# Kernel optimization log

Hardware: AMD Instinct MI355X
Metric: run time of the kernel (lower is better)

Reference implementation:

```python
import jax, jax.numpy as jnp
import numpy as np

B = 128          # batch of trees (same topology)
N_LEAVES = 512
N_NODES = 2 * N_LEAVES - 1   # 1023, null child slot = N_NODES
IN_DIM = 300
MEM_DIM = 300


def _build_tree():
    # complete binary tree, level order: leaves first, then parents.
    null = N_NODES
    left = [null] * N_LEAVES
    right = [null] * N_LEAVES
    prev = list(range(N_LEAVES))
    nid = N_LEAVES
    while len(prev) > 1:
        cur = []
        for k in range(0, len(prev), 2):
            left.append(prev[k]); right.append(prev[k + 1])
            cur.append(nid); nid += 1
        prev = cur
    left = np.asarray(left, np.int32)
    right = np.asarray(right, np.int32)
    leaf_mask = (left == null).astype(np.int32)
    return left, right, leaf_mask


def setup_inputs() -> dict:
    key = jax.random.key(0)
    ks = jax.random.split(key, 5)
    left, right, leaf_mask = _build_tree()
    s = 0.05  # keep gates out of saturation
    return {
        "inputs": jax.random.normal(ks[0], (B, N_NODES, IN_DIM), jnp.float32),
        "Wfioux": jax.random.normal(ks[1], (IN_DIM, 4 * MEM_DIM), jnp.float32) * s,
        "b_fioux": jax.random.normal(ks[2], (4 * MEM_DIM,), jnp.float32) * s,
        "Wiouh": jax.random.normal(ks[3], (2 * MEM_DIM, 3 * MEM_DIM), jnp.float32) * s,
        "Wfh": jax.random.normal(ks[4], (2 * MEM_DIM, 2 * MEM_DIM), jnp.float32) * s,
        "left_idx": jnp.asarray(left),
        "right_idx": jnp.asarray(right),
        "leaf_mask": jnp.asarray(leaf_mask),
    }


def _tree_lstm(inputs, Wfioux, b_fioux, Wiouh, Wfh, left_idx, right_idx, leaf_mask):
    b, n, _ = inputs.shape
    mem = Wiouh.shape[1] // 3
    # internal nodes get zero input (as in the torch code)
    x = inputs * leaf_mask.astype(inputs.dtype)[None, :, None]
    # input-dependent gates precomputed for all nodes: [n, b, 4*mem]
    fioux = jnp.einsum('bni,io->nbo', x, Wfioux) + b_fioux

    C0 = jnp.zeros((n + 1, b, mem), inputs.dtype)  # row n = null child = zeros
    H0 = jnp.zeros((n + 1, b, mem), inputs.dtype)

    def step(carry, xs):
        C, H = carry
        i, li, ri, fioux_i = xs
        ch_c = jnp.concatenate([C[li], C[ri]], axis=-1)  # [b, 2*mem]
        ch_h = jnp.concatenate([H[li], H[ri]], axis=-1)
        fx, ix, ox, ux = jnp.split(fioux_i, 4, axis=-1)
        ih, oh, uh = jnp.split(ch_h @ Wiouh, 3, axis=-1)
        i_g = jax.nn.sigmoid(ix + ih)
        o_g = jax.nn.sigmoid(ox + oh)
        u_g = jnp.tanh(ux + uh)
        f_g = jax.nn.sigmoid(jnp.tile(fx, (1, 2)) + ch_h @ Wfh)
        fc = (f_g * ch_c).reshape(b, 2, mem).sum(axis=1)
        c = i_g * u_g + fc
        h = o_g * jnp.tanh(c)
        return (C.at[li * 0 + i].set(c), H.at[i].set(h)), None

    xs = (jnp.arange(n, dtype=jnp.int32), left_idx, right_idx, fioux)
    (C, H), _ = jax.lax.scan(step, (C0, H0), xs)
    return C[n - 1], H[n - 1]  # root state (c, h), each [b, mem]


def reference(inputs, Wfioux, b_fioux, Wiouh, Wfh, left_idx, right_idx, leaf_mask):
    return _tree_lstm(inputs, Wfioux, b_fioux, Wiouh, Wfh, left_idx, right_idx, leaf_mask)
```

## Files before the change

kernel.cpp:

```cpp
#include <hip/hip_runtime.h>
#include <cstdint>

#define BATCH 128
#define NODES 1023
#define LEAVES 512
#define IN_DIM 300
#define MEM 300
#define NP 320
#define OUT_HALF (BATCH*MEM)

typedef __bf16   bf16x8 __attribute__((ext_vector_type(8)));
typedef short    s16x8  __attribute__((ext_vector_type(8)));
typedef short    s16x4  __attribute__((ext_vector_type(4)));
typedef float    f32x4  __attribute__((ext_vector_type(4)));
typedef _Float16 half_t;

__device__ __forceinline__ short f2bf(float f) {
    unsigned u = __float_as_uint(f);
    u += 0x7fff + ((u >> 16) & 1);
    return (short)(u >> 16);
}
__device__ __forceinline__ float sigf(float x)  { return 1.0f / (1.0f + __expf(-x)); }
__device__ __forceinline__ float tanhf_(float x){ return 1.0f - 2.0f / (1.0f + __expf(2.0f * x)); }

__device__ __forceinline__ f32x4 mfma16(s16x8 a, s16x8 b, f32x4 c) {
    return __builtin_amdgcn_mfma_f32_16x16x32_bf16(
        __builtin_bit_cast(bf16x8, a), __builtin_bit_cast(bf16x8, b), c, 0, 0, 0);
}

__device__ __forceinline__ void dma16(const short* src, short* ldsBase) {
    __builtin_amdgcn_global_load_lds(
        (const __attribute__((address_space(1))) unsigned int*)src,
        (__attribute__((address_space(3))) unsigned int*)ldsBase,
        16, 0, 0);
}

__global__ __launch_bounds__(256) void pack_node_w(
    const float* __restrict__ Wiouh, const float* __restrict__ Wfh, short* __restrict__ Wpk)
{
    int gid = blockIdx.x * 256 + threadIdx.x;
    if (gid >= 2000 * 64) return;
    int fb = gid >> 6, l = gid & 63;
    int kb = fb / 100, rem = fb % 100, s = rem / 20, nb = rem % 20;
    int n = nb * 16 + (l & 15);
    int kbase = kb * 32 + (l >> 4) * 8;
    short v[8];
#pragma unroll
    for (int j = 0; j < 8; ++j) {
        int kp = kbase + j;
        int side = kp >= NP;
        int kk = kp - side * NP;
        float f = 0.0f;
        if (kk < MEM && n < MEM) {
            int k = side * MEM + kk;
            f = (s < 3) ? Wiouh[(size_t)k * 900 + s * 300 + n]
                        : Wfh[(size_t)k * 600 + (s - 3) * 300 + n];
        }
        v[j] = f2bf(f);
    }
    *(s16x8*)&Wpk[(size_t)gid * 8] = *(s16x8*)v;
}

__global__ __launch_bounds__(256) void pack_leaf_w(
    const float* __restrict__ Wfioux, short* __restrict__ Wpk)
{
    int gid = blockIdx.x * 256 + threadIdx.x;
    if (gid >= 600 * 64) return;
    int fb = gid >> 6, l = gid & 63;
    int kb = fb / 60, rem = fb % 60, s = rem / 20, nb = rem % 20;
    int n = nb * 16 + (l & 15);
    int kbase = kb * 32 + (l >> 4) * 8;
    short v[8];
#pragma unroll
    for (int j = 0; j < 8; ++j) {
        int kp = kbase + j;
        float f = 0.0f;
        if (kp < IN_DIM && n < MEM)
            f = Wfioux[(size_t)kp * 1200 + (s + 1) * 300 + n];
        v[j] = f2bf(f);
    }
    *(s16x8*)&Wpk[(size_t)gid * 8] = *(s16x8*)v;
}

__global__ __launch_bounds__(256) void pack_x(
    const float* __restrict__ inputs, short* __restrict__ X)
{
    int gid = blockIdx.x * 256 + threadIdx.x;
    if (gid >= LEAVES * BATCH * (NP / 4)) return;
    int q = gid % (NP / 4);
    int rb = gid / (NP / 4);
    int b = rb % BATCH, leaf = rb / BATCH;
    short v[4] = {0, 0, 0, 0};
    if (q < IN_DIM / 4) {
        f32x4 f = *(const f32x4*)&inputs[((size_t)b * NODES + leaf) * IN_DIM + q * 4];
        v[0] = f2bf(f[0]); v[1] = f2bf(f[1]); v[2] = f2bf(f[2]); v[3] = f2bf(f[3]);
    }
    *(s16x4*)&X[(size_t)gid * 4] = *(s16x4*)v;
}

__global__ __launch_bounds__(256, 3) void leaf_mfma(
    const short* __restrict__ X, const short* __restrict__ Wpk,
    const float* __restrict__ b_fioux, half_t* __restrict__ C, short* __restrict__ H)
{
    __shared__ short Bs[4][12 * 512];
    const int t = threadIdx.x;
    const int l = t & 63, w = t >> 6;
    const int lane16 = l & 15, quad = l >> 4;

    const int bid = blockIdx.x;
    const int xcd = bid & 7, tt = bid >> 3;
    const int y = tt % 5;
    const int leaf = (tt / 5) * 8 + xcd;

    const short* Xb = X + (size_t)leaf * BATCH * NP;

    f32x4 acc[3][4][2];
#pragma unroll
    for (int s = 0; s < 3; ++s)
#pragma unroll
        for (int f = 0; f < 4; ++f)
#pragma unroll
            for (int mi = 0; mi < 2; ++mi) acc[s][f][mi] = (f32x4)(0.0f);

    s16x8 A[4][2];

#define L_STAGE(KB, BUF) do {                                                    \
    _Pragma("unroll")                                                            \
    for (int fl = w; fl < 12; fl += 4) {                                         \
        int s_ = fl >> 2, f_ = fl & 3;                                           \
        const short* src_ = Wpk +                                                \
            ((size_t)(((KB) * 3 + s_) * 20 + y * 4 + f_) * 64 + l) * 8;          \
        dma16(src_, &Bs[BUF][fl * 512]);                                         \
    } } while (0)

#define L_ALOAD(KB, SLOT) do {                                                   \
    const int koff_ = (KB) * 32 + quad * 8;                                      \
    A[SLOT][0] = *(const s16x8*)(Xb + (size_t)(w * 32 + lane16) * NP + koff_);   \
    A[SLOT][1] = *(const s16x8*)(Xb + (size_t)(w * 32 + 16 + lane16) * NP + koff_); \
} while (0)

    L_STAGE(0, 0); L_ALOAD(0, 0);
    L_STAGE(1, 1); L_ALOAD(1, 1);
    L_STAGE(2, 2); L_ALOAD(2, 2);

#define L_STEP(ST, WAITN) do {                                                   \
    asm volatile("s_waitcnt vmcnt(" #WAITN ")" ::: "memory");                    \
    __builtin_amdgcn_s_barrier();                                                \
    asm volatile("" ::: "memory");                                               \
    if ((ST) + 3 < 10) { L_STAGE((ST) + 3, ((ST) + 3) & 3);                      \
                         L_ALOAD((ST) + 3, ((ST) + 3) & 3); }                    \
    _Pragma("unroll")                                                            \
    for (int s_ = 0; s_ < 3; ++s_) {                                             \
        _Pragma("unroll")                                                        \
        for (int f_ = 0; f_ < 4; ++f_) {                                         \
            s16x8 b_ = *(const s16x8*)&Bs[(ST) & 3][(s_ * 4 + f_) * 512 + l * 8];\
            acc[s_][f_][0] = mfma16(A[(ST) & 3][0], b_, acc[s_][f_][0]);         \
            acc[s_][f_][1] = mfma16(A[(ST) & 3][1], b_, acc[s_][f_][1]);         \
        }                                                                        \
    } } while (0)

    L_STEP(0, 10); L_STEP(1, 10); L_STEP(2, 10); L_STEP(3, 10); L_STEP(4, 10);
    L_STEP(5, 10); L_STEP(6, 10); L_STEP(7, 10); L_STEP(8, 5);  L_STEP(9, 0);

#undef L_STEP
#undef L_ALOAD
#undef L_STAGE

#pragma unroll
    for (int f = 0; f < 4; ++f) {
        const int col = y * 64 + f * 16 + lane16;
        const bool valid = col < MEM;
        float bi = 0, bo = 0, bu = 0;
        if (valid) { bi = b_fioux[300 + col]; bo = b_fioux[600 + col]; bu = b_fioux[900 + col]; }
#pragma unroll
        for (int mi = 0; mi < 2; ++mi)
#pragma unroll
            for (int r = 0; r < 4; ++r) {
                int b = w * 32 + mi * 16 + quad * 4 + r;
                size_t hIdx = ((size_t)leaf * BATCH + b) * NP + col;
                if (valid) {
                    float ig = sigf(acc[0][f][mi][r] + bi);
                    float og = sigf(acc[1][f][mi][r] + bo);
                    float ug = tanhf_(acc[2][f][mi][r] + bu);
                    float c = ig * ug;
                    float h = og * tanhf_(c);
                    C[((size_t)leaf * BATCH + b) * MEM + col] = (half_t)c;
                    H[hIdx] = f2bf(h);
                } else {
                    H[hIdx] = 0;
                }
            }
    }
}

__global__ __launch_bounds__(256, 3) void node_mfma(
    const short* __restrict__ Wpk, const float* __restrict__ b_fioux,
    const int* __restrict__ left_idx, const int* __restrict__ right_idx,
    half_t* __restrict__ C, short* __restrict__ H,
    int level_start, int level_size, float* __restrict__ out)
{
    __shared__ short Bs[4][12 * 512];
    const int t = threadIdx.x;
    const int l = t & 63, w = t >> 6;
    const int lane16 = l & 15, quad = l >> 4;

    const int bid = blockIdx.x;
    int nidx, y;
    if ((level_size & 7) == 0) {
        const int xcd = bid & 7, tt = bid >> 3;
        y = tt % 10;
        nidx = (tt / 10) * 8 + xcd;
    } else {
        nidx = bid % level_size;
        y = bid / level_size;
    }
    const int node = level_start + nidx;

    const int li = left_idx[node], ri = right_idx[node];
    const short* HL = H + (size_t)li * BATCH * NP;
    const short* HR = H + (size_t)ri * BATCH * NP;

    f32x4 acc[5][2][2];
#pragma unroll
    for (int s = 0; s < 5; ++s)
#pragma unroll
        for (int f = 0; f < 2; ++f)
#pragma unroll
            for (int mi = 0; mi < 2; ++mi) acc[s][f][mi] = (f32x4)(0.0f);

    s16x8 A[4][2];

#define N_STAGE(KB, BUF) do {                                                    \
    _Pragma("unroll")                                                            \
    for (int fl = w; fl < 12; fl += 4) {                                         \
        int rfl_ = (fl < 10) ? fl : fl - 10;               \
        int s_ = rfl_ >> 1, f_ = rfl_ & 1;                                       \
        const short* src_ = Wpk +                                                \
            ((size_t)(((KB) * 5 + s_) * 20 + y * 2 + f_) * 64 + l) * 8;          \
        dma16(src_, &Bs[BUF][fl * 512]);                                         \
    } } while (0)

#define N_ALOAD(KB, SLOT) do {                                                   \
    const short* Hb_ = (((KB) >= 10) ? HR : HL) +                                \
                       ((KB) - (((KB) >= 10) ? 10 : 0)) * 32 + quad * 8;         \
    A[SLOT][0] = *(const s16x8*)(Hb_ + (size_t)(w * 32 + lane16) * NP);          \
    A[SLOT][1] = *(const s16x8*)(Hb_ + (size_t)(w * 32 + 16 + lane16) * NP);     \
} while (0)

    N_STAGE(0, 0); N_ALOAD(0, 0);
    N_STAGE(1, 1); N_ALOAD(1, 1);
    N_STAGE(2, 2); N_ALOAD(2, 2);

#define N_STEP(ST, WAITN) do {                                                   \
    asm volatile("s_waitcnt vmcnt(" #WAITN ")" ::: "memory");                    \
    __builtin_amdgcn_s_barrier();                                                \
    asm volatile("" ::: "memory");                                               \
    if ((ST) + 3 < 20) { N_STAGE((ST) + 3, ((ST) + 3) & 3);                      \
                         N_ALOAD((ST) + 3, ((ST) + 3) & 3); }                    \
    _Pragma("unroll")                                                            \
    for (int s_ = 0; s_ < 5; ++s_) {                                             \
        _Pragma("unroll")                                                        \
        for (int f_ = 0; f_ < 2; ++f_) {                                         \
            s16x8 b_ = *(const s16x8*)&Bs[(ST) & 3][(s_ * 2 + f_) * 512 + l * 8];\
            acc[s_][f_][0] = mfma16(A[(ST) & 3][0], b_, acc[s_][f_][0]);         \
            acc[s_][f_][1] = mfma16(A[(ST) & 3][1], b_, acc[s_][f_][1]);         \
        }                                                                        \
    } } while (0)

    N_STEP(0, 10);  N_STEP(1, 10);  N_STEP(2, 10);  N_STEP(3, 10);  N_STEP(4, 10);
    N_STEP(5, 10);  N_STEP(6, 10);  N_STEP(7, 10);  N_STEP(8, 10);  N_STEP(9, 10);
    N_STEP(10, 10); N_STEP(11, 10); N_STEP(12, 10); N_STEP(13, 10); N_STEP(14, 10);
    N_STEP(15, 10); N_STEP(16, 10); N_STEP(17, 10); N_STEP(18, 5);  N_STEP(19, 0);

#undef N_STEP
#undef N_ALOAD
#undef N_STAGE

#pragma unroll
    for (int f = 0; f < 2; ++f) {
        const int col = y * 32 + f * 16 + lane16;
        const bool valid = col < MEM;
        float bff = 0, bi = 0, bo = 0, bu = 0;
        if (valid) {
            bff = b_fioux[col]; bi = b_fioux[300 + col];
            bo = b_fioux[600 + col]; bu = b_fioux[900 + col];
        }
#pragma unroll
        for (int mi = 0; mi < 2; ++mi)
#pragma unroll
            for (int r = 0; r < 4; ++r) {
                int row = w * 32 + mi * 16 + quad * 4 + r;
                size_t hIdx = ((size_t)node * BATCH + row) * NP + col;
                if (valid) {
                    float cl = (float)C[((size_t)li * BATCH + row) * MEM + col];
                    float cr = (float)C[((size_t)ri * BATCH + row) * MEM + col];
                    float ig = sigf(acc[0][f][mi][r] + bi);
                    float og = sigf(acc[1][f][mi][r] + bo);
                    float ug = tanhf_(acc[2][f][mi][r] + bu);
                    float fl = sigf(acc[3][f][mi][r] + bff);
                    float fr = sigf(acc[4][f][mi][r] + bff);
                    float c = ig * ug + fl * cl + fr * cr;
                    float h = og * tanhf_(c);
                    C[((size_t)node * BATCH + row) * MEM + col] = (half_t)c;
                    H[hIdx] = f2bf(h);
                    if (out) {
                        out[row * MEM + col] = c;
                        out[OUT_HALF + row * MEM + col] = h;
                    }
                } else {
                    H[hIdx] = 0;
                }
            }
    }
}

extern "C" void kernel_launch(void* const* d_in, const int* in_sizes, int n_in,
                              void* d_out, int out_size, void* d_ws, size_t ws_size,
                              hipStream_t stream) {
    const float* inputs  = (const float*)d_in[0];
    const float* Wfioux  = (const float*)d_in[1];
    const float* b_fioux = (const float*)d_in[2];
    const float* Wiouh   = (const float*)d_in[3];
    const float* Wfh     = (const float*)d_in[4];
    const int*   left_idx  = (const int*)d_in[5];
    const int*   right_idx = (const int*)d_in[6];

    half_t* C   = (half_t*)d_ws;
    short*  H   = (short*)(C + (size_t)NODES * BATCH * MEM);
    short* WpkN = H + (size_t)NODES * BATCH * NP;
    short* WpkL = WpkN + (size_t)2000 * 512;
    short* X    = WpkL + (size_t)600 * 512;
    float* out  = (float*)d_out;

    pack_x<<<(LEAVES * BATCH * (NP / 4) + 255) / 256, 256, 0, stream>>>(inputs, X);
    pack_leaf_w<<<150, 256, 0, stream>>>(Wfioux, WpkL);
    pack_node_w<<<500, 256, 0, stream>>>(Wiouh, Wfh, WpkN);

    leaf_mfma<<<LEAVES * 5, 256, 0, stream>>>(X, WpkL, b_fioux, C, H);

    static const int starts[9] = {512, 768, 896, 960, 992, 1008, 1016, 1020, 1022};
    static const int sizes [9] = {256, 128,  64,  32,  16,    8,    4,    2,    1};
    for (int lvl = 0; lvl < 9; ++lvl) {
        bool root = (lvl == 8);
        node_mfma<<<sizes[lvl] * 10, 256, 0, stream>>>(
            WpkN, b_fioux, left_idx, right_idx, C, H, starts[lvl], sizes[lvl],
            root ? out : nullptr);
    }
}
```

Measured before the change: 627.8 us.

## Split waves 2x2 over rows and columns, shorten A-fragment prefetch depth

Each kernel's four waves are rearranged from four row-slices (each covering all columns) into a 2x2 grid: each wave now handles 64 batch rows and half of the block's columns. Each wave therefore reads half as many B fragments from LDS per MFMA but loads twice as many A rows from global memory. The A-operand global prefetch drops from three stages ahead to one (double buffer), while the LDS weight staging keeps three stages ahead, and the vmcnt wait counts are retuned to match. This is meant to cut LDS read traffic and register pressure, at the risk of exposing more global load latency on the A operand.

Result: slower. 798.2 us (+27.1%).

```diff
diff --git a/kernel.cpp b/kernel.cpp
--- a/kernel.cpp
+++ b/kernel.cpp
@@ -106,6 +106,7 @@
     const int t = threadIdx.x;
     const int l = t & 63, w = t >> 6;
     const int lane16 = l & 15, quad = l >> 4;
+    const int mw = w >> 1, nw = w & 1;
 
     const int bid = blockIdx.x;
     const int xcd = bid & 7, tt = bid >> 3;
@@ -114,15 +115,15 @@
 
     const short* Xb = X + (size_t)leaf * BATCH * NP;
 
-    f32x4 acc[3][4][2];
+    f32x4 acc[3][2][4];
 #pragma unroll
     for (int s = 0; s < 3; ++s)
 #pragma unroll
-        for (int f = 0; f < 4; ++f)
-#pragma unroll
-            for (int mi = 0; mi < 2; ++mi) acc[s][f][mi] = (f32x4)(0.0f);
-
-    s16x8 A[4][2];
+        for (int fh = 0; fh < 2; ++fh)
+#pragma unroll
+            for (int rh = 0; rh < 4; ++rh) acc[s][fh][rh] = (f32x4)(0.0f);
+
+    s16x8 A[2][4];
 
 #define L_STAGE(KB, BUF) do {                                                    \
     _Pragma("unroll")                                                            \
@@ -135,53 +136,56 @@
 
 #define L_ALOAD(KB, SLOT) do {                                                   \
     const int koff_ = (KB) * 32 + quad * 8;                                      \
-    A[SLOT][0] = *(const s16x8*)(Xb + (size_t)(w * 32 + lane16) * NP + koff_);   \
-    A[SLOT][1] = *(const s16x8*)(Xb + (size_t)(w * 32 + 16 + lane16) * NP + koff_); \
+    _Pragma("unroll")                                                            \
+    for (int rh_ = 0; rh_ < 4; ++rh_)                                            \
+        A[SLOT][rh_] = *(const s16x8*)(Xb +                                      \
+            (size_t)(mw * 64 + rh_ * 16 + lane16) * NP + koff_);                 \
 } while (0)
 
-    L_STAGE(0, 0); L_ALOAD(0, 0);
-    L_STAGE(1, 1); L_ALOAD(1, 1);
-    L_STAGE(2, 2); L_ALOAD(2, 2);
+    L_ALOAD(0, 0);
+    L_STAGE(0, 0); L_STAGE(1, 1); L_STAGE(2, 2);
 
 #define L_STEP(ST, WAITN) do {                                                   \
     asm volatile("s_waitcnt vmcnt(" #WAITN ")" ::: "memory");                    \
     __builtin_amdgcn_s_barrier();                                                \
     asm volatile("" ::: "memory");                                               \
-    if ((ST) + 3 < 10) { L_STAGE((ST) + 3, ((ST) + 3) & 3);                      \
-                         L_ALOAD((ST) + 3, ((ST) + 3) & 3); }                    \
+    if ((ST) + 1 < 10) L_ALOAD((ST) + 1, ((ST) + 1) & 1);                        \
+    if ((ST) + 3 < 10) L_STAGE((ST) + 3, ((ST) + 3) & 3);                        \
     _Pragma("unroll")                                                            \
     for (int s_ = 0; s_ < 3; ++s_) {                                             \
         _Pragma("unroll")                                                        \
-        for (int f_ = 0; f_ < 4; ++f_) {                                         \
-            s16x8 b_ = *(const s16x8*)&Bs[(ST) & 3][(s_ * 4 + f_) * 512 + l * 8];\
-            acc[s_][f_][0] = mfma16(A[(ST) & 3][0], b_, acc[s_][f_][0]);         \
-            acc[s_][f_][1] = mfma16(A[(ST) & 3][1], b_, acc[s_][f_][1]);         \
+        for (int fh_ = 0; fh_ < 2; ++fh_) {                                      \
+            s16x8 b_ = *(const s16x8*)                                           \
+                &Bs[(ST) & 3][(s_ * 4 + nw * 2 + fh_) * 512 + l * 8];            \
+            _Pragma("unroll")                                                    \
+            for (int rh_ = 0; rh_ < 4; ++rh_)                                    \
+                acc[s_][fh_][rh_] = mfma16(A[(ST) & 1][rh_], b_, acc[s_][fh_][rh_]); \
         }                                                                        \
     } } while (0)
 
-    L_STEP(0, 10); L_STEP(1, 10); L_STEP(2, 10); L_STEP(3, 10); L_STEP(4, 10);
-    L_STEP(5, 10); L_STEP(6, 10); L_STEP(7, 10); L_STEP(8, 5);  L_STEP(9, 0);
+    L_STEP(0, 6); L_STEP(1, 3); L_STEP(2, 3); L_STEP(3, 3); L_STEP(4, 3);
+    L_STEP(5, 3); L_STEP(6, 3); L_STEP(7, 3); L_STEP(8, 0); L_STEP(9, 0);
 
 #undef L_STEP
 #undef L_ALOAD
 #undef L_STAGE
 
 #pragma unroll
-    for (int f = 0; f < 4; ++f) {
-        const int col = y * 64 + f * 16 + lane16;
+    for (int fh = 0; fh < 2; ++fh) {
+        const int col = y * 64 + (nw * 2 + fh) * 16 + lane16;
         const bool valid = col < MEM;
         float bi = 0, bo = 0, bu = 0;
         if (valid) { bi = b_fioux[300 + col]; bo = b_fioux[600 + col]; bu = b_fioux[900 + col]; }
 #pragma unroll
-        for (int mi = 0; mi < 2; ++mi)
+        for (int rh = 0; rh < 4; ++rh)
 #pragma unroll
             for (int r = 0; r < 4; ++r) {
-                int b = w * 32 + mi * 16 + quad * 4 + r;
+                int b = mw * 64 + rh * 16 + quad * 4 + r;
                 size_t hIdx = ((size_t)leaf * BATCH + b) * NP + col;
                 if (valid) {
-                    float ig = sigf(acc[0][f][mi][r] + bi);
-                    float og = sigf(acc[1][f][mi][r] + bo);
-                    float ug = tanhf_(acc[2][f][mi][r] + bu);
+                    float ig = sigf(acc[0][fh][rh][r] + bi);
+                    float og = sigf(acc[1][fh][rh][r] + bo);
+                    float ug = tanhf_(acc[2][fh][rh][r] + bu);
                     float c = ig * ug;
                     float h = og * tanhf_(c);
                     C[((size_t)leaf * BATCH + b) * MEM + col] = (half_t)c;
@@ -203,6 +207,7 @@
     const int t = threadIdx.x;
     const int l = t & 63, w = t >> 6;
     const int lane16 = l & 15, quad = l >> 4;
+    const int mw = w >> 1, nw = w & 1;
 
     const int bid = blockIdx.x;
     int nidx, y;
@@ -220,15 +225,13 @@
     const short* HL = H + (size_t)li * BATCH * NP;
     const short* HR = H + (size_t)ri * BATCH * NP;
 
-    f32x4 acc[5][2][2];
+    f32x4 acc[5][4];
 #pragma unroll
     for (int s = 0; s < 5; ++s)
 #pragma unroll
-        for (int f = 0; f < 2; ++f)
-#pragma unroll
-            for (int mi = 0; mi < 2; ++mi) acc[s][f][mi] = (f32x4)(0.0f);
-
-    s16x8 A[4][2];
+        for (int rh = 0; rh < 4; ++rh) acc[s][rh] = (f32x4)(0.0f);
+
+    s16x8 A[2][4];
 
 #define N_STAGE(KB, BUF) do {                                                    \
     _Pragma("unroll")                                                            \
@@ -243,42 +246,41 @@
 #define N_ALOAD(KB, SLOT) do {                                                   \
     const short* Hb_ = (((KB) >= 10) ? HR : HL) +                                \
                        ((KB) - (((KB) >= 10) ? 10 : 0)) * 32 + quad * 8;         \
-    A[SLOT][0] = *(const s16x8*)(Hb_ + (size_t)(w * 32 + lane16) * NP);          \
-    A[SLOT][1] = *(const s16x8*)(Hb_ + (size_t)(w * 32 + 16 + lane16) * NP);     \
+    _Pragma("unroll")                                                            \
+    for (int rh_ = 0; rh_ < 4; ++rh_)                                            \
+        A[SLOT][rh_] = *(const s16x8*)(Hb_ +                                     \
+            (size_t)(mw * 64 + rh_ * 16 + lane16) * NP);                         \
 } while (0)
 
-    N_STAGE(0, 0); N_ALOAD(0, 0);
-    N_STAGE(1, 1); N_ALOAD(1, 1);
-    N_STAGE(2, 2); N_ALOAD(2, 2);
+    N_ALOAD(0, 0);
+    N_STAGE(0, 0); N_STAGE(1, 1); N_STAGE(2, 2);
 
 #define N_STEP(ST, WAITN) do {                                                   \
     asm volatile("s_waitcnt vmcnt(" #WAITN ")" ::: "memory");                    \
     __builtin_amdgcn_s_barrier();                                                \
     asm volatile("" ::: "memory");                                               \
-    if ((ST) + 3 < 20) { N_STAGE((ST) + 3, ((ST) + 3) & 3);                      \
-                         N_ALOAD((ST) + 3, ((ST) + 3) & 3); }                    \
+    if ((ST) + 1 < 20) N_ALOAD((ST) + 1, ((ST) + 1) & 1);                        \
+    if ((ST) + 3 < 20) N_STAGE((ST) + 3, ((ST) + 3) & 3);                        \
     _Pragma("unroll")                                                            \
     for (int s_ = 0; s_ < 5; ++s_) {                                             \
+        s16x8 b_ = *(const s16x8*)                                               \
+            &Bs[(ST) & 3][(s_ * 2 + nw) * 512 + l * 8];                          \
         _Pragma("unroll")                                                        \
-        for (int f_ = 0; f_ < 2; ++f_) {                                         \
-            s16x8 b_ = *(const s16x8*)&Bs[(ST) & 3][(s_ * 2 + f_) * 512 + l * 8];\
-            acc[s_][f_][0] = mfma16(A[(ST) & 3][0], b_, acc[s_][f_][0]);         \
-            acc[s_][f_][1] = mfma16(A[(ST) & 3][1], b_, acc[s_][f_][1]);         \
-        }                                                                        \
+        for (int rh_ = 0; rh_ < 4; ++rh_)                                        \
+            acc[s_][rh_] = mfma16(A[(ST) & 1][rh_], b_, acc[s_][rh_]);           \
     } } while (0)
 
-    N_STEP(0, 10);  N_STEP(1, 10);  N_STEP(2, 10);  N_STEP(3, 10);  N_STEP(4, 10);
-    N_STEP(5, 10);  N_STEP(6, 10);  N_STEP(7, 10);  N_STEP(8, 10);  N_STEP(9, 10);
-    N_STEP(10, 10); N_STEP(11, 10); N_STEP(12, 10); N_STEP(13, 10); N_STEP(14, 10);
-    N_STEP(15, 10); N_STEP(16, 10); N_STEP(17, 10); N_STEP(18, 5);  N_STEP(19, 0);
+    N_STEP(0, 6);   N_STEP(1, 3);   N_STEP(2, 3);   N_STEP(3, 3);   N_STEP(4, 3);
+    N_STEP(5, 3);   N_STEP(6, 3);   N_STEP(7, 3);   N_STEP(8, 3);   N_STEP(9, 3);
+    N_STEP(10, 3);  N_STEP(11, 3);  N_STEP(12, 3);  N_STEP(13, 3);  N_STEP(14, 3);
+    N_STEP(15, 3);  N_STEP(16, 3);  N_STEP(17, 3);  N_STEP(18, 0);  N_STEP(19, 0);
 
 #undef N_STEP
 #undef N_ALOAD
 #undef N_STAGE
 
-#pragma unroll
-    for (int f = 0; f < 2; ++f) {
-        const int col = y * 32 + f * 16 + lane16;
+    {
+        const int col = y * 32 + nw * 16 + lane16;
         const bool valid = col < MEM;
         float bff = 0, bi = 0, bo = 0, bu = 0;
         if (valid) {
@@ -286,19 +288,19 @@
             bo = b_fioux[600 + col]; bu = b_fioux[900 + col];
         }
 #pragma unroll
-        for (int mi = 0; mi < 2; ++mi)
+        for (int rh = 0; rh < 4; ++rh)
 #pragma unroll
             for (int r = 0; r < 4; ++r) {
-                int row = w * 32 + mi * 16 + quad * 4 + r;
+                int row = mw * 64 + rh * 16 + quad * 4 + r;
                 size_t hIdx = ((size_t)node * BATCH + row) * NP + col;
                 if (valid) {
                     float cl = (float)C[((size_t)li * BATCH + row) * MEM + col];
                     float cr = (float)C[((size_t)ri * BATCH + row) * MEM + col];
-                    float ig = sigf(acc[0][f][mi][r] + bi);
-                    float og = sigf(acc[1][f][mi][r] + bo);
-                    float ug = tanhf_(acc[2][f][mi][r] + bu);
-                    float fl = sigf(acc[3][f][mi][r] + bff);
-                    float fr = sigf(acc[4][f][mi][r] + bff);
+                    float ig = sigf(acc[0][rh][r] + bi);
+                    float og = sigf(acc[1][rh][r] + bo);
+                    float ug = tanhf_(acc[2][rh][r] + bu);
+                    float fl = sigf(acc[3][rh][r] + bff);
+                    float fr = sigf(acc[4][rh][r] + bff);
                     float c = ig * ug + fl * cl + fr * cr;
                     float h = og * tanhf_(c);
                     C[((size_t)node * BATCH + row) * MEM + col] = (half_t)c;
```

## Fuse input bf16 packing into leaf MFMA kernel and halve column tile

Applied to the files above, without the earlier changes.

Drops the separate pack_x pass. The leaf kernel now loads fp32 leaf inputs straight from the input tensor and converts them to bf16 in registers, masking the K-padding tail on the last step. Column tiles per block shrink from 64 to 32, so the grid doubles to 10 blocks per leaf and the LDS stage buffers get smaller. This removes a full write and re-read of the packed intermediate. In exchange, each block reads fp32 data (twice the bytes), rereads it across 10 column blocks, and does the conversion inside the pipelined loop.

New measurement: 647.8 us. 1.03x slower.

```diff
diff --git a/kernel.cpp b/kernel.cpp
--- a/kernel.cpp
+++ b/kernel.cpp
@@ -33,6 +33,22 @@
         (const __attribute__((address_space(1))) unsigned int*)src,
         (__attribute__((address_space(3))) unsigned int*)ldsBase,
         16, 0, 0);
+}
+
+__device__ __forceinline__ s16x8 cvt8f(f32x4 lo, f32x4 hi) {
+    s16x8 r;
+#pragma unroll
+    for (int j = 0; j < 4; ++j) { r[j] = f2bf(lo[j]); r[4 + j] = f2bf(hi[j]); }
+    return r;
+}
+__device__ __forceinline__ s16x8 cvt8m(f32x4 lo, f32x4 hi, int koff) {
+    s16x8 r;
+#pragma unroll
+    for (int j = 0; j < 4; ++j) {
+        r[j]     = (koff + j     < IN_DIM) ? f2bf(lo[j]) : (short)0;
+        r[4 + j] = (koff + 4 + j < IN_DIM) ? f2bf(hi[j]) : (short)0;
+    }
+    return r;
 }
 
 __global__ __launch_bounds__(256) void pack_node_w(
@@ -82,61 +98,50 @@
     *(s16x8*)&Wpk[(size_t)gid * 8] = *(s16x8*)v;
 }
 
-__global__ __launch_bounds__(256) void pack_x(
-    const float* __restrict__ inputs, short* __restrict__ X)
-{
-    int gid = blockIdx.x * 256 + threadIdx.x;
-    if (gid >= LEAVES * BATCH * (NP / 4)) return;
-    int q = gid % (NP / 4);
-    int rb = gid / (NP / 4);
-    int b = rb % BATCH, leaf = rb / BATCH;
-    short v[4] = {0, 0, 0, 0};
-    if (q < IN_DIM / 4) {
-        f32x4 f = *(const f32x4*)&inputs[((size_t)b * NODES + leaf) * IN_DIM + q * 4];
-        v[0] = f2bf(f[0]); v[1] = f2bf(f[1]); v[2] = f2bf(f[2]); v[3] = f2bf(f[3]);
-    }
-    *(s16x4*)&X[(size_t)gid * 4] = *(s16x4*)v;
-}
-
 __global__ __launch_bounds__(256, 3) void leaf_mfma(
-    const short* __restrict__ X, const short* __restrict__ Wpk,
+    const float* __restrict__ inputs, const short* __restrict__ Wpk,
     const float* __restrict__ b_fioux, half_t* __restrict__ C, short* __restrict__ H)
 {
-    __shared__ short Bs[4][12 * 512];
+    __shared__ short Bs[4][8 * 512];
     const int t = threadIdx.x;
     const int l = t & 63, w = t >> 6;
     const int lane16 = l & 15, quad = l >> 4;
 
     const int bid = blockIdx.x;
     const int xcd = bid & 7, tt = bid >> 3;
-    const int y = tt % 5;
-    const int leaf = (tt / 5) * 8 + xcd;
-
-    const short* Xb = X + (size_t)leaf * BATCH * NP;
-
-    f32x4 acc[3][4][2];
+    const int y = tt % 10;
+    const int leaf = (tt / 10) * 8 + xcd;
+
+    f32x4 acc[3][2][2];
 #pragma unroll
     for (int s = 0; s < 3; ++s)
 #pragma unroll
-        for (int f = 0; f < 4; ++f)
+        for (int f = 0; f < 2; ++f)
 #pragma unroll
             for (int mi = 0; mi < 2; ++mi) acc[s][f][mi] = (f32x4)(0.0f);
 
-    s16x8 A[4][2];
+    f32x4 Af[4][2][2];
 
 #define L_STAGE(KB, BUF) do {                                                    \
     _Pragma("unroll")                                                            \
-    for (int fl = w; fl < 12; fl += 4) {                                         \
-        int s_ = fl >> 2, f_ = fl & 3;                                           \
+    for (int fl = w * 2; fl < w * 2 + 2; ++fl) {                                 \
+        int rfl_ = (fl < 6) ? fl : fl - 6;                                       \
+        int s_ = rfl_ >> 1, f_ = rfl_ & 1;                                       \
         const short* src_ = Wpk +                                                \
-            ((size_t)(((KB) * 3 + s_) * 20 + y * 4 + f_) * 64 + l) * 8;          \
+            ((size_t)(((KB) * 3 + s_) * 20 + y * 2 + f_) * 64 + l) * 8;          \
         dma16(src_, &Bs[BUF][fl * 512]);                                         \
     } } while (0)
 
 #define L_ALOAD(KB, SLOT) do {                                                   \
     const int koff_ = (KB) * 32 + quad * 8;                                      \
-    A[SLOT][0] = *(const s16x8*)(Xb + (size_t)(w * 32 + lane16) * NP + koff_);   \
-    A[SLOT][1] = *(const s16x8*)(Xb + (size_t)(w * 32 + 16 + lane16) * NP + koff_); \
+    const float* p0_ = inputs +                                                  \
+        ((size_t)(w * 32 + lane16) * NODES + leaf) * IN_DIM + koff_;             \
+    const float* p1_ = inputs +                                                  \
+        ((size_t)(w * 32 + 16 + lane16) * NODES + leaf) * IN_DIM + koff_;        \
+    Af[SLOT][0][0] = *(const f32x4*)(p0_);                                       \
+    Af[SLOT][0][1] = *(const f32x4*)(p0_ + 4);                                   \
+    Af[SLOT][1][0] = *(const f32x4*)(p1_);                                       \
+    Af[SLOT][1][1] = *(const f32x4*)(p1_ + 4);                                   \
 } while (0)
 
     L_STAGE(0, 0); L_ALOAD(0, 0);
@@ -149,26 +154,35 @@
     asm volatile("" ::: "memory");                                               \
     if ((ST) + 3 < 10) { L_STAGE((ST) + 3, ((ST) + 3) & 3);                      \
                          L_ALOAD((ST) + 3, ((ST) + 3) & 3); }                    \
+    s16x8 a0_, a1_;                                                              \
+    if ((ST) < 9) {                                                              \
+        a0_ = cvt8f(Af[(ST) & 3][0][0], Af[(ST) & 3][0][1]);                     \
+        a1_ = cvt8f(Af[(ST) & 3][1][0], Af[(ST) & 3][1][1]);                     \
+    } else {                                                                     \
+        const int ko_ = (ST) * 32 + quad * 8;                                    \
+        a0_ = cvt8m(Af[(ST) & 3][0][0], Af[(ST) & 3][0][1], ko_);                \
+        a1_ = cvt8m(Af[(ST) & 3][1][0], Af[(ST) & 3][1][1], ko_);                \
+    }                                                                            \
     _Pragma("unroll")                                                            \
     for (int s_ = 0; s_ < 3; ++s_) {                                             \
         _Pragma("unroll")                                                        \
-        for (int f_ = 0; f_ < 4; ++f_) {                                         \
-            s16x8 b_ = *(const s16x8*)&Bs[(ST) & 3][(s_ * 4 + f_) * 512 + l * 8];\
-            acc[s_][f_][0] = mfma16(A[(ST) & 3][0], b_, acc[s_][f_][0]);         \
-            acc[s_][f_][1] = mfma16(A[(ST) & 3][1], b_, acc[s_][f_][1]);         \
+        for (int f_ = 0; f_ < 2; ++f_) {                                         \
+            s16x8 b_ = *(const s16x8*)&Bs[(ST) & 3][(s_ * 2 + f_) * 512 + l * 8];\
+            acc[s_][f_][0] = mfma16(a0_, b_, acc[s_][f_][0]);                    \
+            acc[s_][f_][1] = mfma16(a1_, b_, acc[s_][f_][1]);                    \
         }                                                                        \
     } } while (0)
 
-    L_STEP(0, 10); L_STEP(1, 10); L_STEP(2, 10); L_STEP(3, 10); L_STEP(4, 10);
-    L_STEP(5, 10); L_STEP(6, 10); L_STEP(7, 10); L_STEP(8, 5);  L_STEP(9, 0);
+    L_STEP(0, 12); L_STEP(1, 12); L_STEP(2, 12); L_STEP(3, 12); L_STEP(4, 12);
+    L_STEP(5, 12); L_STEP(6, 12); L_STEP(7, 12); L_STEP(8, 6);  L_STEP(9, 0);
 
 #undef L_STEP
 #undef L_ALOAD
 #undef L_STAGE
 
 #pragma unroll
-    for (int f = 0; f < 4; ++f) {
-        const int col = y * 64 + f * 16 + lane16;
+    for (int f = 0; f < 2; ++f) {
+        const int col = y * 32 + f * 16 + lane16;
         const bool valid = col < MEM;
         float bi = 0, bo = 0, bu = 0;
         if (valid) { bi = b_fioux[300 + col]; bo = b_fioux[600 + col]; bu = b_fioux[900 + col]; }
@@ -329,14 +343,12 @@
     short*  H   = (short*)(C + (size_t)NODES * BATCH * MEM);
     short* WpkN = H + (size_t)NODES * BATCH * NP;
     short* WpkL = WpkN + (size_t)2000 * 512;
-    short* X    = WpkL + (size_t)600 * 512;
     float* out  = (float*)d_out;
 
-    pack_x<<<(LEAVES * BATCH * (NP / 4) + 255) / 256, 256, 0, stream>>>(inputs, X);
     pack_leaf_w<<<150, 256, 0, stream>>>(Wfioux, WpkL);
     pack_node_w<<<500, 256, 0, stream>>>(Wiouh, Wfh, WpkN);
 
-    leaf_mfma<<<LEAVES * 5, 256, 0, stream>>>(X, WpkL, b_fioux, C, H);
+    leaf_mfma<<<LEAVES * 10, 256, 0, stream>>>(inputs, WpkL, b_fioux, C, H);
 
     static const int starts[9] = {512, 768, 896, 960, 992, 1008, 1016, 1020, 1022};
     static const int sizes [9] = {256, 128,  64,  32,  16,    8,    4,    2,    1};
```

## Store X and H in k-block-major blocked layout for coalesced MFMA A-loads

Applied to the files above, without the earlier changes.

Changes the packed input X and hidden state H from row-major [row][320] to a blocked layout [kblock of 8][batch][8], so each quad's 16-byte A-operand loads for consecutive lanes become contiguous. The leaf and node kernels' A-loads and H stores are rewritten to match, and pack_x now writes 8-element chunks. This targets strided, poorly coalesced global reads of A fragments, at the cost of scattered 2-byte H stores in the epilogue.

Result: no change. 632.0 us (+0.7%).

```diff
diff --git a/kernel.cpp b/kernel.cpp
--- a/kernel.cpp
+++ b/kernel.cpp
@@ -7,11 +7,12 @@
 #define IN_DIM 300
 #define MEM 300
 #define NP 320
+#define KB_CNT 40
+#define HNODE (KB_CNT*BATCH*8)
 #define OUT_HALF (BATCH*MEM)
 
 typedef __bf16   bf16x8 __attribute__((ext_vector_type(8)));
 typedef short    s16x8  __attribute__((ext_vector_type(8)));
-typedef short    s16x4  __attribute__((ext_vector_type(4)));
 typedef float    f32x4  __attribute__((ext_vector_type(4)));
 typedef _Float16 half_t;
 
@@ -82,20 +83,22 @@
     *(s16x8*)&Wpk[(size_t)gid * 8] = *(s16x8*)v;
 }
 
-__global__ __launch_bounds__(256) void pack_x(
+__global__ __launch_bounds__(256) void pack_x2(
     const float* __restrict__ inputs, short* __restrict__ X)
 {
     int gid = blockIdx.x * 256 + threadIdx.x;
-    if (gid >= LEAVES * BATCH * (NP / 4)) return;
-    int q = gid % (NP / 4);
-    int rb = gid / (NP / 4);
+    if (gid >= LEAVES * BATCH * KB_CNT) return;
+    int kb = gid % KB_CNT;
+    int rb = gid / KB_CNT;
     int b = rb % BATCH, leaf = rb / BATCH;
-    short v[4] = {0, 0, 0, 0};
-    if (q < IN_DIM / 4) {
-        f32x4 f = *(const f32x4*)&inputs[((size_t)b * NODES + leaf) * IN_DIM + q * 4];
-        v[0] = f2bf(f[0]); v[1] = f2bf(f[1]); v[2] = f2bf(f[2]); v[3] = f2bf(f[3]);
-    }
-    *(s16x4*)&X[(size_t)gid * 4] = *(s16x4*)v;
+    const float* src = inputs + ((size_t)b * NODES + leaf) * IN_DIM + kb * 8;
+    short v[8];
+#pragma unroll
+    for (int j = 0; j < 8; ++j) {
+        int k = kb * 8 + j;
+        v[j] = (k < IN_DIM) ? f2bf(src[j]) : (short)0;
+    }
+    *(s16x8*)&X[(size_t)((leaf * KB_CNT + kb) * BATCH + b) * 8] = *(s16x8*)v;
 }
 
 __global__ __launch_bounds__(256, 3) void leaf_mfma(
@@ -112,7 +115,7 @@
     const int y = tt % 5;
     const int leaf = (tt / 5) * 8 + xcd;
 
-    const short* Xb = X + (size_t)leaf * BATCH * NP;
+    const short* Xb = X + (size_t)leaf * HNODE;
 
     f32x4 acc[3][4][2];
 #pragma unroll
@@ -134,9 +137,9 @@
     } } while (0)
 
 #define L_ALOAD(KB, SLOT) do {                                                   \
-    const int koff_ = (KB) * 32 + quad * 8;                                      \
-    A[SLOT][0] = *(const s16x8*)(Xb + (size_t)(w * 32 + lane16) * NP + koff_);   \
-    A[SLOT][1] = *(const s16x8*)(Xb + (size_t)(w * 32 + 16 + lane16) * NP + koff_); \
+    const short* p_ = Xb + (size_t)(((KB) * 4 + quad) * BATCH + w * 32 + lane16) * 8; \
+    A[SLOT][0] = *(const s16x8*)(p_);                                            \
+    A[SLOT][1] = *(const s16x8*)(p_ + 16 * 8);                                   \
 } while (0)
 
     L_STAGE(0, 0); L_ALOAD(0, 0);
@@ -177,7 +180,8 @@
 #pragma unroll
             for (int r = 0; r < 4; ++r) {
                 int b = w * 32 + mi * 16 + quad * 4 + r;
-                size_t hIdx = ((size_t)leaf * BATCH + b) * NP + col;
+                size_t hIdx = (size_t)leaf * HNODE +
+                              (size_t)((col >> 3) * BATCH + b) * 8 + (col & 7);
                 if (valid) {
                     float ig = sigf(acc[0][f][mi][r] + bi);
                     float og = sigf(acc[1][f][mi][r] + bo);
@@ -217,8 +221,8 @@
     const int node = level_start + nidx;
 
     const int li = left_idx[node], ri = right_idx[node];
-    const short* HL = H + (size_t)li * BATCH * NP;
-    const short* HR = H + (size_t)ri * BATCH * NP;
+    const short* HL = H + (size_t)li * HNODE;
+    const short* HR = H + (size_t)ri * HNODE;
 
     f32x4 acc[5][2][2];
 #pragma unroll
@@ -241,10 +245,12 @@
     } } while (0)
 
 #define N_ALOAD(KB, SLOT) do {                                                   \
-    const short* Hb_ = (((KB) >= 10) ? HR : HL) +                                \
-                       ((KB) - (((KB) >= 10) ? 10 : 0)) * 32 + quad * 8;         \
-    A[SLOT][0] = *(const s16x8*)(Hb_ + (size_t)(w * 32 + lane16) * NP);          \
-    A[SLOT][1] = *(const s16x8*)(Hb_ + (size_t)(w * 32 + 16 + lane16) * NP);     \
+    const short* Hb_ = ((KB) >= 10) ? HR : HL;                                   \
+    const int kb32_ = (KB) - (((KB) >= 10) ? 10 : 0);                            \
+    const short* p_ = Hb_ +                                                      \
+        (size_t)((kb32_ * 4 + quad) * BATCH + w * 32 + lane16) * 8;              \
+    A[SLOT][0] = *(const s16x8*)(p_);                                            \
+    A[SLOT][1] = *(const s16x8*)(p_ + 16 * 8);                                   \
 } while (0)
 
     N_STAGE(0, 0); N_ALOAD(0, 0);
@@ -290,7 +296,8 @@
 #pragma unroll
             for (int r = 0; r < 4; ++r) {
                 int row = w * 32 + mi * 16 + quad * 4 + r;
-                size_t hIdx = ((size_t)node * BATCH + row) * NP + col;
+                size_t hIdx = (size_t)node * HNODE +
+                              (size_t)((col >> 3) * BATCH + row) * 8 + (col & 7);
                 if (valid) {
                     float cl = (float)C[((size_t)li * BATCH + row) * MEM + col];
                     float cr = (float)C[((size_t)ri * BATCH + row) * MEM + col];
@@ -327,12 +334,12 @@
 
     half_t* C   = (half_t*)d_ws;
     short*  H   = (short*)(C + (size_t)NODES * BATCH * MEM);
-    short* WpkN = H + (size_t)NODES * BATCH * NP;
+    short* WpkN = H + (size_t)NODES * HNODE;
     short* WpkL = WpkN + (size_t)2000 * 512;
     short* X    = WpkL + (size_t)600 * 512;
     float* out  = (float*)d_out;
 
-    pack_x<<<(LEAVES * BATCH * (NP / 4) + 255) / 256, 256, 0, stream>>>(inputs, X);
+    pack_x2<<<(LEAVES * BATCH * KB_CNT + 255) / 256, 256, 0, stream>>>(inputs, X);
     pack_leaf_w<<<150, 256, 0, stream>>>(Wfioux, WpkL);
     pack_node_w<<<500, 256, 0, stream>>>(Wiouh, Wfh, WpkN);
 
```
